# Kernel tuning notes

Measured on AMD Instinct MI355X. Metric: run time of the kernel, lower is better.

The kernel has to match this reference:

```python
import jax, jax.numpy as jnp
import numpy as np

N_QUBITS = 4
N_LAYERS = 2
BATCH = 262144


def _apply_ry(psi, theta, wire):
    # psi: (B, 2,2,2,2) real statevector; theta: scalar or (B,)
    c = jnp.reshape(jnp.cos(theta * 0.5), (-1, 1, 1, 1))
    s = jnp.reshape(jnp.sin(theta * 0.5), (-1, 1, 1, 1))
    psi = jnp.moveaxis(psi, wire + 1, 1)
    a, b = psi[:, 0], psi[:, 1]
    psi = jnp.stack([c * a - s * b, s * a + c * b], axis=1)
    return jnp.moveaxis(psi, 1, wire + 1)


def _apply_cnot(psi, ctrl, tgt):
    # flip target amplitude where control bit is 1
    psi = jnp.moveaxis(psi, (ctrl + 1, tgt + 1), (1, 2))
    psi = psi.at[:, 1].set(psi[:, 1, ::-1])
    return jnp.moveaxis(psi, (1, 2), (ctrl + 1, tgt + 1))


def _circuit(encoded, q_params):
    # Batched 4-qubit statevector sim (RY/CNOT are real matrices -> real psi).
    B = encoded.shape[0]
    psi = jnp.zeros((B, 2 ** N_QUBITS), encoded.dtype).at[:, 0].set(1.0)
    psi = psi.reshape((B,) + (2,) * N_QUBITS)  # wire 0 = most significant axis
    for w in range(N_QUBITS):
        psi = _apply_ry(psi, encoded[:, w], w)
    for layer in range(N_LAYERS):
        for i in range(N_QUBITS - 1):
            psi = _apply_cnot(psi, i, i + 1)
        psi = _apply_cnot(psi, N_QUBITS - 1, 0)  # ring closure (n_qubits > 2)
        for i in range(N_QUBITS):
            psi = _apply_ry(psi, q_params[layer * N_QUBITS + i], i)
    p = psi * psi  # probabilities
    zs = []
    for w in range(N_QUBITS):
        pw = jnp.moveaxis(p, w + 1, 1).reshape(B, 2, -1)
        zs.append(pw[:, 0].sum(-1) - pw[:, 1].sum(-1))  # <Z_w>
    return jnp.stack(zs, axis=-1)  # (B, 4)


def setup_inputs() -> dict:
    key = jax.random.key(0)
    ks = jax.random.split(key, 10)
    f32 = jnp.float32
    state = jax.random.normal(ks[0], (BATCH, 64), dtype=f32)
    # state_encoder: Linear(64,32) -> ReLU -> Linear(32,4) -> Tanh
    W1 = jax.random.normal(ks[1], (32, 64), dtype=f32) / np.sqrt(64.0)
    b1 = jnp.zeros((32,), f32)
    W2 = jax.random.normal(ks[2], (N_QUBITS, 32), dtype=f32) / np.sqrt(32.0)
    b2 = jnp.zeros((N_QUBITS,), f32)
    q_params = jax.random.normal(ks[3], (N_LAYERS * N_QUBITS,), dtype=f32) * 0.1
    # q_value_head: Linear(4,32) -> ReLU -> Linear(32,16) -> Tanh
    H1 = jax.random.normal(ks[4], (32, N_QUBITS), dtype=f32) / np.sqrt(float(N_QUBITS))
    c1 = jnp.zeros((32,), f32)
    H2 = jax.random.normal(ks[5], (16, 32), dtype=f32) / np.sqrt(32.0)
    c2 = jnp.zeros((16,), f32)
    return {"state": state, "W1": W1, "b1": b1, "W2": W2, "b2": b2,
            "q_params": q_params, "H1": H1, "c1": c1, "H2": H2, "c2": c2}


def reference(state, W1, b1, W2, b2, q_params, H1, c1, H2, c2):
    B = state.shape[0]
    x = state.reshape(B, -1)
    h = jax.nn.relu(x @ W1.T + b1)
    encoded = jnp.tanh(h @ W2.T + b2)            # (B, 4) rotation angles
    qf = _circuit(encoded, q_params)             # (B, 4) PauliZ expectations
    h2 = jax.nn.relu(qf @ H1.T + c1)
    q_values = jnp.tanh(h2 @ H2.T + c2)          # (B, 16)
    return q_values.reshape(B, 4, 4)
```

## Files before the change

### kernel.cpp

```cpp
#include <hip/hip_runtime.h>
#include <hip/hip_bf16.h>

#define TPB 256
#define BATCH 262144
#define S 34

typedef __fp16   fp16x2  __attribute__((ext_vector_type(2)));
typedef _Float16 half8_t __attribute__((ext_vector_type(8)));
typedef float    f32x4   __attribute__((ext_vector_type(4)));

#define WAVE_LDS_FENCE() asm volatile("s_waitcnt lgkmcnt(0)" ::: "memory")

__device__ __forceinline__ float fast_tanh(float x) {
    float ax = fabsf(x);
    float e  = __expf(-2.0f * ax);
    float t  = (1.0f - e) * __builtin_amdgcn_rcpf(1.0f + e);
    return copysignf(t, x);
}

template <int MASK>
__device__ __forceinline__ void ry_gate(float* psi, float c, float s) {
#pragma unroll
    for (int i = 0; i < 16; i++) {
        if (!(i & MASK)) {
            float a = psi[i], b = psi[i | MASK];
            psi[i]        = c * a - s * b;
            psi[i | MASK] = s * a + c * b;
        }
    }
}

template <int CM, int TM>
__device__ __forceinline__ void cnot_gate(float* psi) {
#pragma unroll
    for (int i = 0; i < 16; i++) {
        if ((i & CM) && !(i & TM)) {
            float t = psi[i];
            psi[i] = psi[i | TM];
            psi[i | TM] = t;
        }
    }
}

__device__ __forceinline__ half8_t cvt8(float4 a, float4 b) {
    fp16x2 p0 = __builtin_amdgcn_cvt_pkrtz(a.x, a.y);
    fp16x2 p1 = __builtin_amdgcn_cvt_pkrtz(a.z, a.w);
    fp16x2 p2 = __builtin_amdgcn_cvt_pkrtz(b.x, b.y);
    fp16x2 p3 = __builtin_amdgcn_cvt_pkrtz(b.z, b.w);
    half8_t r;
    r[0] = (_Float16)p0[0]; r[1] = (_Float16)p0[1];
    r[2] = (_Float16)p1[0]; r[3] = (_Float16)p1[1];
    r[4] = (_Float16)p2[0]; r[5] = (_Float16)p2[1];
    r[6] = (_Float16)p3[0]; r[7] = (_Float16)p3[1];
    return r;
}

__global__ __launch_bounds__(TPB, 4) void qnet_kernel(
    const float* __restrict__ state,
    const float* __restrict__ W1, const float* __restrict__ b1,
    const float* __restrict__ W2, const float* __restrict__ b2,
    const float* __restrict__ qp,
    const float* __restrict__ H1, const float* __restrict__ c1,
    const float* __restrict__ H2, const float* __restrict__ c2,
    float* __restrict__ out)
{
    __shared__ float sh[4 * 64 * S];

    const int tid  = threadIdx.x;
    const int lane = tid & 63;
    const int wv   = tid >> 6;
    const int l15  = lane & 15;
    const int lq   = lane >> 4;
    const int rowBase = blockIdx.x * TPB + wv * 64;
    float* hb = sh + wv * 64 * S;

    float4 xa[4][2], xb[4][2];
#pragma unroll
    for (int mt = 0; mt < 4; mt++) {
        const float* p0 = state + (size_t)(rowBase + 16 * mt + l15) * 64 + lq * 8;
#pragma unroll
        for (int kt = 0; kt < 2; kt++) {
            xa[mt][kt] = *(const float4*)(p0 + 32 * kt);
            xb[mt][kt] = *(const float4*)(p0 + 32 * kt + 4);
        }
    }

    half8_t bW1[2][2];
#pragma unroll
    for (int u = 0; u < 2; u++)
#pragma unroll
        for (int kt = 0; kt < 2; kt++) {
            const float* p = W1 + (16 * u + l15) * 64 + 32 * kt + lq * 8;
            bW1[u][kt] = cvt8(*(const float4*)p, *(const float4*)(p + 4));
        }
    const float bias0 = b1[l15];
    const float bias1 = b1[16 + l15];

    f32x4 acc[4][2];
#pragma unroll
    for (int mt = 0; mt < 4; mt++)
#pragma unroll
        for (int u = 0; u < 2; u++)
#pragma unroll
            for (int r = 0; r < 4; r++) acc[mt][u][r] = 0.0f;

#pragma unroll
    for (int kt = 0; kt < 2; kt++) {
#pragma unroll
        for (int mt = 0; mt < 4; mt++) {
            half8_t a = cvt8(xa[mt][kt], xb[mt][kt]);
            acc[mt][0] = __builtin_amdgcn_mfma_f32_16x16x32_f16(a, bW1[0][kt], acc[mt][0], 0, 0, 0);
            acc[mt][1] = __builtin_amdgcn_mfma_f32_16x16x32_f16(a, bW1[1][kt], acc[mt][1], 0, 0, 0);
        }
    }

#pragma unroll
    for (int mt = 0; mt < 4; mt++)
#pragma unroll
        for (int r = 0; r < 4; r++) {
            int row = 16 * mt + 4 * lq + r;
            hb[row * S + l15]      = fmaxf(acc[mt][0][r] + bias0, 0.0f);
            hb[row * S + 16 + l15] = fmaxf(acc[mt][1][r] + bias1, 0.0f);
        }
    WAVE_LDS_FENCE();

    float h[32];
    {
        const float2* hr = reinterpret_cast<const float2*>(hb + lane * S);
#pragma unroll
        for (int j = 0; j < 16; j++) { float2 v = hr[j]; h[2 * j] = v.x; h[2 * j + 1] = v.y; }
    }

    float e[4];
#pragma unroll
    for (int w = 0; w < 4; w++) {
        float a = b2[w];
#pragma unroll
        for (int k = 0; k < 32; k++) a = fmaf(h[k], W2[w * 32 + k], a);
        e[w] = fast_tanh(a);
    }

    float qf[4];
    {
        float psi[16];
#pragma unroll
        for (int i = 0; i < 16; i++) psi[i] = 0.0f;
        psi[0] = 1.0f;

        float s, c;
        __sincosf(0.5f * e[0], &s, &c); ry_gate<8>(psi, c, s);
        __sincosf(0.5f * e[1], &s, &c); ry_gate<4>(psi, c, s);
        __sincosf(0.5f * e[2], &s, &c); ry_gate<2>(psi, c, s);
        __sincosf(0.5f * e[3], &s, &c); ry_gate<1>(psi, c, s);

#pragma unroll
        for (int layer = 0; layer < 2; layer++) {
            cnot_gate<8, 4>(psi);
            cnot_gate<4, 2>(psi);
            cnot_gate<2, 1>(psi);
            cnot_gate<1, 8>(psi);
#pragma unroll
            for (int i = 0; i < 4; i++) {
                float s2, c2v;
                __sincosf(0.5f * qp[layer * 4 + i], &s2, &c2v);
                if (i == 0) ry_gate<8>(psi, c2v, s2);
                if (i == 1) ry_gate<4>(psi, c2v, s2);
                if (i == 2) ry_gate<2>(psi, c2v, s2);
                if (i == 3) ry_gate<1>(psi, c2v, s2);
            }
        }

        float p[16];
#pragma unroll
        for (int i = 0; i < 16; i++) p[i] = psi[i] * psi[i];
#pragma unroll
        for (int w = 0; w < 4; w++) {
            const int m = 8 >> w;
            float z = 0.0f;
#pragma unroll
            for (int i = 0; i < 16; i++) z += (i & m) ? -p[i] : p[i];
            qf[w] = z;
        }
    }

    float h2[32];
#pragma unroll
    for (int j = 0; j < 32; j++) {
        float a = c1[j];
        a = fmaf(qf[0], H1[j * 4 + 0], a);
        a = fmaf(qf[1], H1[j * 4 + 1], a);
        a = fmaf(qf[2], H1[j * 4 + 2], a);
        a = fmaf(qf[3], H1[j * 4 + 3], a);
        h2[j] = fmaxf(a, 0.0f);
    }

    WAVE_LDS_FENCE();
    {
        float2* hw = reinterpret_cast<float2*>(hb + lane * S);
#pragma unroll
        for (int j = 0; j < 16; j++) hw[j] = make_float2(h2[2 * j], h2[2 * j + 1]);
    }
    WAVE_LDS_FENCE();

    half8_t bH2;
    {
        const float* p = H2 + l15 * 32 + lq * 8;
        bH2 = cvt8(*(const float4*)p, *(const float4*)(p + 4));
    }

    f32x4 acc2[4];
#pragma unroll
    for (int mt = 0; mt < 4; mt++)
#pragma unroll
        for (int r = 0; r < 4; r++) acc2[mt][r] = 0.0f;

#pragma unroll
    for (int mt = 0; mt < 4; mt++) {
        const float2* q = reinterpret_cast<const float2*>(hb + (16 * mt + l15) * S + lq * 8);
        float2 a0 = q[0], a1 = q[1], a2 = q[2], a3 = q[3];
        half8_t a = cvt8(make_float4(a0.x, a0.y, a1.x, a1.y),
                         make_float4(a2.x, a2.y, a3.x, a3.y));
        acc2[mt] = __builtin_amdgcn_mfma_f32_16x16x32_f16(a, bH2, acc2[mt], 0, 0, 0);
    }

    const float cc = c2[l15];
#pragma unroll
    for (int mt = 0; mt < 4; mt++)
#pragma unroll
        for (int r = 0; r < 4; r++) {
            int row = rowBase + 16 * mt + 4 * lq + r;
            out[(size_t)row * 16 + l15] = fast_tanh(acc2[mt][r] + cc);
        }
}

extern "C" void kernel_launch(void* const* d_in, const int* in_sizes, int n_in,
                              void* d_out, int out_size, void* d_ws, size_t ws_size,
                              hipStream_t stream) {
    const float* state = (const float*)d_in[0];
    const float* W1    = (const float*)d_in[1];
    const float* b1    = (const float*)d_in[2];
    const float* W2    = (const float*)d_in[3];
    const float* b2    = (const float*)d_in[4];
    const float* qp    = (const float*)d_in[5];
    const float* H1    = (const float*)d_in[6];
    const float* c1    = (const float*)d_in[7];
    const float* H2    = (const float*)d_in[8];
    const float* c2    = (const float*)d_in[9];
    float* out = (float*)d_out;

    const int blocks = BATCH / TPB;
    qnet_kernel<<<blocks, TPB, 0, stream>>>(state, W1, b1, W2, b2, qp,
                                            H1, c1, H2, c2, out);
}
```

Before: 119.8 us.

## Compute encoder second layer with MFMA and simplify circuit state init and reductions

Replaces the per-thread 32x4 scalar dot product (which needed 32 LDS reads per lane) with a 16x16x32 f16 MFMA over the hidden tile, then transposes the 4 outputs through LDS. Builds the initial product state directly from sin/cos tensor products instead of four RY gate passes, and rewrites the PauliZ reductions with shared partial sums. The h2 activations are also stored in LDS as packed fp16, which halves LDS traffic before the second MFMA. The trade-off is extra LDS round trips and fences, plus fp16 rounding of the encoder layer, which could affect accuracy.

```diff
diff --git a/kernel.cpp b/kernel.cpp
--- a/kernel.cpp
+++ b/kernel.cpp
@@ -1,9 +1,10 @@
 #include <hip/hip_runtime.h>
-#include <hip/hip_bf16.h>
 
 #define TPB 256
 #define BATCH 262144
 #define S 34
+#define EST 10
+#define H2ST 36
 
 typedef __fp16   fp16x2  __attribute__((ext_vector_type(2)));
 typedef _Float16 half8_t __attribute__((ext_vector_type(8)));
@@ -55,6 +56,13 @@
     return r;
 }
 
+__device__ __forceinline__ half8_t cvt8_rne(float4 a, float4 b) {
+    half8_t r;
+    r[0] = (_Float16)a.x; r[1] = (_Float16)a.y; r[2] = (_Float16)a.z; r[3] = (_Float16)a.w;
+    r[4] = (_Float16)b.x; r[5] = (_Float16)b.y; r[6] = (_Float16)b.z; r[7] = (_Float16)b.w;
+    return r;
+}
+
 __global__ __launch_bounds__(TPB, 4) void qnet_kernel(
     const float* __restrict__ state,
     const float* __restrict__ W1, const float* __restrict__ b1,
@@ -124,34 +132,53 @@
         }
     WAVE_LDS_FENCE();
 
-    float h[32];
-    {
-        const float2* hr = reinterpret_cast<const float2*>(hb + lane * S);
-#pragma unroll
-        for (int j = 0; j < 16; j++) { float2 v = hr[j]; h[2 * j] = v.x; h[2 * j + 1] = v.y; }
-    }
+    half8_t bW2;
+    {
+        const float* p = W2 + (l15 & 3) * 32 + lq * 8;
+        bW2 = cvt8_rne(*(const float4*)p, *(const float4*)(p + 4));
+    }
+    f32x4 eacc[4];
+#pragma unroll
+    for (int mt = 0; mt < 4; mt++) {
+#pragma unroll
+        for (int r = 0; r < 4; r++) eacc[mt][r] = 0.0f;
+        const float2* q = reinterpret_cast<const float2*>(hb + (16 * mt + l15) * S + lq * 8);
+        float2 a0 = q[0], a1 = q[1], a2 = q[2], a3 = q[3];
+        half8_t a = cvt8_rne(make_float4(a0.x, a0.y, a1.x, a1.y),
+                             make_float4(a2.x, a2.y, a3.x, a3.y));
+        eacc[mt] = __builtin_amdgcn_mfma_f32_16x16x32_f16(a, bW2, eacc[mt], 0, 0, 0);
+    }
+    WAVE_LDS_FENCE();
+
+    if (l15 < 4) {
+#pragma unroll
+        for (int mt = 0; mt < 4; mt++)
+#pragma unroll
+            for (int r = 0; r < 4; r++)
+                hb[(16 * mt + 4 * lq + r) * EST + l15] = eacc[mt][r];
+    }
+    WAVE_LDS_FENCE();
 
     float e[4];
-#pragma unroll
-    for (int w = 0; w < 4; w++) {
-        float a = b2[w];
-#pragma unroll
-        for (int k = 0; k < 32; k++) a = fmaf(h[k], W2[w * 32 + k], a);
-        e[w] = fast_tanh(a);
+    {
+        const float2* ep = reinterpret_cast<const float2*>(hb + lane * EST);
+        float2 v0 = ep[0], v1 = ep[1];
+        e[0] = fast_tanh(v0.x + b2[0]);
+        e[1] = fast_tanh(v0.y + b2[1]);
+        e[2] = fast_tanh(v1.x + b2[2]);
+        e[3] = fast_tanh(v1.y + b2[3]);
     }
 
     float qf[4];
     {
+        float sn[4], cs[4];
+#pragma unroll
+        for (int w = 0; w < 4; w++) __sincosf(0.5f * e[w], &sn[w], &cs[w]);
+        float t01[4] = { cs[0]*cs[1], cs[0]*sn[1], sn[0]*cs[1], sn[0]*sn[1] };
+        float t23[4] = { cs[2]*cs[3], cs[2]*sn[3], sn[2]*cs[3], sn[2]*sn[3] };
         float psi[16];
 #pragma unroll
-        for (int i = 0; i < 16; i++) psi[i] = 0.0f;
-        psi[0] = 1.0f;
-
-        float s, c;
-        __sincosf(0.5f * e[0], &s, &c); ry_gate<8>(psi, c, s);
-        __sincosf(0.5f * e[1], &s, &c); ry_gate<4>(psi, c, s);
-        __sincosf(0.5f * e[2], &s, &c); ry_gate<2>(psi, c, s);
-        __sincosf(0.5f * e[3], &s, &c); ry_gate<1>(psi, c, s);
+        for (int i = 0; i < 16; i++) psi[i] = t01[i >> 2] * t23[i & 3];
 
 #pragma unroll
         for (int layer = 0; layer < 2; layer++) {
@@ -170,20 +197,25 @@
             }
         }
 
-        float p[16];
-#pragma unroll
-        for (int i = 0; i < 16; i++) p[i] = psi[i] * psi[i];
-#pragma unroll
-        for (int w = 0; w < 4; w++) {
-            const int m = 8 >> w;
-            float z = 0.0f;
-#pragma unroll
-            for (int i = 0; i < 16; i++) z += (i & m) ? -p[i] : p[i];
-            qf[w] = z;
-        }
-    }
-
-    float h2[32];
+        float p_[16];
+#pragma unroll
+        for (int i = 0; i < 16; i++) p_[i] = psi[i] * psi[i];
+        float d0 = p_[0] - p_[8],  d1 = p_[1] - p_[9];
+        float d2 = p_[2] - p_[10], d3 = p_[3] - p_[11];
+        float d4 = p_[4] - p_[12], d5 = p_[5] - p_[13];
+        float d6 = p_[6] - p_[14], d7 = p_[7] - p_[15];
+        qf[0] = ((d0 + d1) + (d2 + d3)) + ((d4 + d5) + (d6 + d7));
+        float s0 = p_[0] + p_[8],  s1 = p_[1] + p_[9];
+        float s2 = p_[2] + p_[10], s3 = p_[3] + p_[11];
+        float s4 = p_[4] + p_[12], s5 = p_[5] + p_[13];
+        float s6 = p_[6] + p_[14], s7 = p_[7] + p_[15];
+        qf[1] = ((s0 - s4) + (s1 - s5)) + ((s2 - s6) + (s3 - s7));
+        float u0 = s0 + s4, u1 = s1 + s5, u2 = s2 + s6, u3 = s3 + s7;
+        qf[2] = (u0 - u2) + (u1 - u3);
+        qf[3] = (u0 + u2) - (u1 + u3);
+    }
+
+    float h2v[32];
 #pragma unroll
     for (int j = 0; j < 32; j++) {
         float a = c1[j];
@@ -191,14 +223,19 @@
         a = fmaf(qf[1], H1[j * 4 + 1], a);
         a = fmaf(qf[2], H1[j * 4 + 2], a);
         a = fmaf(qf[3], H1[j * 4 + 3], a);
-        h2[j] = fmaxf(a, 0.0f);
-    }
-
-    WAVE_LDS_FENCE();
-    {
-        float2* hw = reinterpret_cast<float2*>(hb + lane * S);
-#pragma unroll
-        for (int j = 0; j < 16; j++) hw[j] = make_float2(h2[2 * j], h2[2 * j + 1]);
+        h2v[j] = fmaxf(a, 0.0f);
+    }
+
+    {
+        uint2* wp = reinterpret_cast<uint2*>(
+            reinterpret_cast<__fp16*>(hb) + (size_t)lane * H2ST);
+#pragma unroll
+        for (int j = 0; j < 8; j++) {
+            fp16x2 q0 = __builtin_amdgcn_cvt_pkrtz(h2v[4 * j],     h2v[4 * j + 1]);
+            fp16x2 q1 = __builtin_amdgcn_cvt_pkrtz(h2v[4 * j + 2], h2v[4 * j + 3]);
+            wp[j] = make_uint2(__builtin_bit_cast(unsigned int, q0),
+                               __builtin_bit_cast(unsigned int, q1));
+        }
     }
     WAVE_LDS_FENCE();
 
@@ -210,16 +247,14 @@
 
     f32x4 acc2[4];
 #pragma unroll
-    for (int mt = 0; mt < 4; mt++)
+    for (int mt = 0; mt < 4; mt++) {
 #pragma unroll
         for (int r = 0; r < 4; r++) acc2[mt][r] = 0.0f;
-
-#pragma unroll
-    for (int mt = 0; mt < 4; mt++) {
-        const float2* q = reinterpret_cast<const float2*>(hb + (16 * mt + l15) * S + lq * 8);
-        float2 a0 = q[0], a1 = q[1], a2 = q[2], a3 = q[3];
-        half8_t a = cvt8(make_float4(a0.x, a0.y, a1.x, a1.y),
-                         make_float4(a2.x, a2.y, a3.x, a3.y));
+        const __fp16* rp = reinterpret_cast<const __fp16*>(hb)
+                         + (16 * mt + l15) * H2ST + lq * 8;
+        uint2 wlo = *reinterpret_cast<const uint2*>(rp);
+        uint2 whi = *reinterpret_cast<const uint2*>(rp + 4);
+        half8_t a = __builtin_bit_cast(half8_t, make_uint4(wlo.x, wlo.y, whi.x, whi.y));
         acc2[mt] = __builtin_amdgcn_mfma_f32_16x16x32_f16(a, bH2, acc2[mt], 0, 0, 0);
     }
 
```

Measured after the change: 122.1 us. No clear change (+1.9%).
